# Kernel optimization log

Hardware: AMD Instinct MI355X
Metric: run time of the kernel (lower is better)

The kernel has to match this reference:

```python
import jax, jax.numpy as jnp
import numpy as np

MAX_DELAY = 48          # delay buffer depth
D1 = MAX_DELAY + 1
SIGMA = MAX_DELAY / 2.0
MAX_THINK = 8           # config.max_think_steps
NUM_CLASSES = 63
VOCAB = NUM_CLASSES + 1 # vocab includes think-end token
THINK_END = NUM_CLASSES
H = 512                 # hidden_size
B = 8                   # batch
T = 48                  # encoder time steps


def _calc_credit(tau):
    # relu(-|(d - clip(tau,1,D)) * (1/sigma)^2| + 1/sigma), shape (D1,H,H)
    tc = jnp.clip(tau, 1.0, float(MAX_DELAY))[None]
    d = jnp.arange(D1, dtype=tau.dtype)[:, None, None]
    inv = 1.0 / SIGMA
    return jax.nn.relu(inv - jnp.abs((d - tc) * (inv * inv)))


def _forward(x, wa, ba, lat, tau, we, be, N):
    cm = _calc_credit(tau) * lat[None]   # (D1,H,H), constant across steps
    d_idx = jnp.arange(D1)

    def step_b(buf, ptr, x_t):           # buf (D1,Bx,H), x_t (Bx,VOCAB)
        h_del = jax.lax.dynamic_index_in_dim(buf, ptr, 0, keepdims=False)
        h = jnp.tanh(x_t @ wa.T + ba + h_del)
        scat = jnp.einsum('dhi,bi->dbh', cm, h)
        shifted = scat[(d_idx - ptr) % D1]                      # roll by +ptr along d
        buf = (buf + shifted) * (d_idx != ptr).astype(buf.dtype)[:, None, None]
        y = h_del @ we.T + be
        return buf, (ptr + 1) % D1, y

    def step_1(buf, ptr, x_t):           # per-sample: buf (D1,H), x_t (VOCAB,)
        h_del = jax.lax.dynamic_index_in_dim(buf, ptr, 0, keepdims=False)
        h = jnp.tanh(wa @ x_t + ba + h_del)
        scat = jnp.einsum('dhi,i->dh', cm, h)
        shifted = scat[(d_idx - ptr) % D1]
        buf = (buf + shifted) * (d_idx != ptr).astype(buf.dtype)[:, None]
        y = we @ h_del + be
        return buf, (ptr + 1) % D1, y

    def gumbel_hard(y, k):               # F.gumbel_softmax(tau=1, hard=True)
        u = jax.random.uniform(k, y.shape, minval=1e-9, maxval=1.0)
        logits = y - jnp.log(-jnp.log(u))
        soft = jax.nn.softmax(logits)
        idx = jnp.argmax(logits)
        hard = jax.nn.one_hot(idx, VOCAB, dtype=y.dtype)
        return hard + soft - jax.lax.stop_gradient(soft), idx

    bsz = x.shape[0]
    buf0 = jnp.zeros((D1, bsz, H), x.dtype)

    def enc(carry, x_t):
        buf, ptr = carry
        buf, ptr, _ = step_b(buf, ptr, x_t)
        return (buf, ptr), None

    (buf, ptr), _ = jax.lax.scan(enc, (buf0, jnp.int32(0)), jnp.swapaxes(x, 0, 1))

    def decode_one(buf_i, x_last, key_i):
        # bounded think loop (original while-loop, max MAX_THINK+1 iterations)
        def think(carry, i):
            b, cur, p, done = carry
            nb, np_, y = step_1(b, p, cur)
            ncur, idx = gumbel_hard(y, jax.random.fold_in(key_i, i))
            b = jnp.where(done, b, nb)
            cur = jnp.where(done, cur, ncur)
            p = jnp.where(done, p, np_)
            done = done | (idx == THINK_END) | (i + 1 > MAX_THINK)
            return (b, cur, p, done), None
        (b, cur, p, _), _ = jax.lax.scan(
            think, (buf_i, x_last, ptr, jnp.bool_(False)), jnp.arange(MAX_THINK + 1))

        def dec(carry, j):
            b, cur, p = carry
            b, p, y = step_1(b, p, cur)
            ncur, _ = gumbel_hard(y, jax.random.fold_in(key_i, 10000 + j))
            return (b, ncur, p), y
        _, ys = jax.lax.scan(dec, (b, cur, p), jnp.arange(N))
        return ys                        # (N, VOCAB)

    keys = jax.random.split(jax.random.key(42), bsz)
    ys = jax.vmap(decode_one, in_axes=(1, 0, 0))(buf, x[:, -1, :], keys)
    return ys[:, :, :-1]                 # drop think-end logit


def setup_inputs() -> dict:
    key = jax.random.key(0)
    ks = jax.random.split(key, 6)
    x = jax.random.normal(ks[0], (B, T, VOCAB), dtype=jnp.float32)
    lim_a = (6.0 / (VOCAB + H)) ** 0.5
    w_afferent = jax.random.uniform(ks[1], (H, VOCAB), minval=-lim_a, maxval=lim_a)
    b_afferent = jnp.zeros((H,), jnp.float32)
    lim_l = (6.0 / (H + H)) ** 0.5
    lateral = jax.random.uniform(ks[2], (H, H), minval=-lim_l, maxval=lim_l)
    tau = MAX_DELAY * jax.random.uniform(ks[3], (H, H)) + 1.0
    lim_e = (6.0 / (H + VOCAB)) ** 0.5
    w_efferent = jax.random.uniform(ks[4], (VOCAB, H), minval=-lim_e, maxval=lim_e)
    b_efferent = jnp.zeros((VOCAB,), jnp.float32)
    return {"x": x, "w_afferent": w_afferent, "b_afferent": b_afferent,
            "lateral": lateral, "tau": tau,
            "w_efferent": w_efferent, "b_efferent": b_efferent, "N": T - 3}


def reference(x, w_afferent, b_afferent, lateral, tau, w_efferent, b_efferent, N):
    return _forward(x, w_afferent, b_afferent, lateral, tau, w_efferent, b_efferent, N)
```

## Files before the change

### kernel.cpp

```cpp
#include <hip/hip_runtime.h>
#include <stdint.h>

namespace {

constexpr int H = 512, V = 64, B = 8, T = 48, D1 = 49, NDEC = 45, NSTEP = 102;
constexpr int NBLK = 256, TPB = 512;
constexpr int NG = 8, GMEM = NBLK / NG;

constexpr size_t OFF_PUB  = 0;
constexpr size_t OFF_IDX  = 131072;
constexpr size_t OFF_PFLG = 132096;
constexpr size_t OFF_YPF  = 132352;
constexpr size_t OFF_YF   = 132416;
constexpr size_t OFF_BAR  = 132544;
constexpr size_t OFF_YP   = 133056;
constexpr size_t OFF_XW   = 149440;

__device__ __forceinline__ float ldA(const float* p) {
  return __hip_atomic_load(p, __ATOMIC_RELAXED, __HIP_MEMORY_SCOPE_AGENT);
}
__device__ __forceinline__ void stA(float* p, float v) {
  __hip_atomic_store(p, v, __ATOMIC_RELAXED, __HIP_MEMORY_SCOPE_AGENT);
}
__device__ __forceinline__ int ldAi(const int* p) {
  return __hip_atomic_load(p, __ATOMIC_RELAXED, __HIP_MEMORY_SCOPE_AGENT);
}
__device__ __forceinline__ void stAi(int* p, int v) {
  __hip_atomic_store(p, v, __ATOMIC_RELAXED, __HIP_MEMORY_SCOPE_AGENT);
}

__device__ __forceinline__ void tf2x32(uint32_t k0, uint32_t k1,
                                       uint32_t& x0, uint32_t& x1) {
  const uint32_t ks2 = k0 ^ k1 ^ 0x1BD11BDAu;
  x0 += k0; x1 += k1;
#define RR(r) { x0 += x1; x1 = (x1 << (r)) | (x1 >> (32-(r))); x1 ^= x0; }
  RR(13) RR(15) RR(26) RR(6)  x0 += k1;  x1 += ks2 + 1u;
  RR(17) RR(29) RR(16) RR(24) x0 += ks2; x1 += k0 + 2u;
  RR(13) RR(15) RR(26) RR(6)  x0 += k0;  x1 += k1 + 3u;
  RR(17) RR(29) RR(16) RR(24) x0 += k1;  x1 += ks2 + 4u;
  RR(13) RR(15) RR(26) RR(6)  x0 += ks2; x1 += k0 + 5u;
#undef RR
}

__device__ __forceinline__ float gumbel_from_bits(uint32_t bits) {
  float u = __uint_as_float((bits >> 9) | 0x3F800000u) - 1.0f;
  u = u + 1e-9f;
  return -logf(-logf(u));
}

__global__ __launch_bounds__(512) void k_zero(float* __restrict__ ws) {
  int* ib = (int*)ws;
  for (size_t i = OFF_PFLG + threadIdx.x; i < OFF_BAR + 512; i += 512)
    stAi(&ib[i], 0);
  for (int i = threadIdx.x; i < 32768; i += 512) stA(&ws[i], 0.0f);
}

__device__ __forceinline__ void gbar(int* bar, int grp, int ep) {
  asm volatile("s_waitcnt vmcnt(0)" ::: "memory");
  __syncthreads();
  if (threadIdx.x == 0) {
    int old = __hip_atomic_fetch_add(&bar[16 + 16 * grp], 1,
                                     __ATOMIC_RELAXED, __HIP_MEMORY_SCOPE_AGENT);
    if (((old + 1) & (GMEM - 1)) == 0) {
      int oldG = __hip_atomic_fetch_add(&bar[0], 1,
                                        __ATOMIC_RELAXED, __HIP_MEMORY_SCOPE_AGENT);
      if (((oldG + 1) & (NG - 1)) == 0) {
        #pragma unroll
        for (int q = 0; q < NG; ++q) stAi(&bar[160 + 16 * q], ep);
      }
    }
    int guard = 0;
    while (ldAi(&bar[160 + 16 * grp]) < ep) {
      __builtin_amdgcn_s_sleep(2);
      if (++guard > (1 << 20)) break;
    }
  }
  __syncthreads();
}

__global__ __launch_bounds__(TPB, 4)
void k_main(
    const float* __restrict__ x,  const float* __restrict__ wa,
    const float* __restrict__ ba, const float* __restrict__ lat,
    const float* __restrict__ tau,const float* __restrict__ we,
    const float* __restrict__ be, float* __restrict__ ws,
    float* __restrict__ out) {
  const int blk = blockIdx.x, tid = threadIdx.x;
  float* pub = ws + OFF_PUB;
  float* yp  = ws + OFF_YP;
  float* xw  = ws + OFF_XW;
  int* idxA  = (int*)ws + OFF_IDX;
  int* pflag = (int*)ws + OFF_PFLG;
  int* ypf   = (int*)ws + OFF_YPF;
  int* yf    = (int*)ws + OFF_YF;
  int* bar   = (int*)ws + OFF_BAR;

  const int p  = blk >> 5;
  const int g  = blk & 31;
  const int w  = tid >> 6, lane = tid & 63;
  const int cb = p * 64;
  const bool isG0  = (g == 0);
  const bool isFin = (g == 31);
  const int fb = p;

  __shared__ float s_h[8 * 64];
  __shared__ float s_hd2[8 * 64];
  __shared__ float s_tc[16 * 64];
  __shared__ float s_lat[16 * 64];
  __shared__ float s_buf[8 * 16 * 49];
  __shared__ int   s_ptr[8], s_cidx[8], s_done8[8];

  for (int q2 = tid; q2 < 8 * 16 * 49; q2 += TPB) s_buf[q2] = 0.0f;
  for (int q2 = tid; q2 < 16 * 64; q2 += TPB) {
    int hl = q2 >> 6, ii = q2 & 63;
    int ho = g * 16 + hl, i = cb + ii;
    float tv = tau[(size_t)ho * H + i];
    s_tc[q2]  = fminf(fmaxf(tv, 1.0f), 48.0f);
    s_lat[q2] = lat[(size_t)ho * H + i];
  }
  if (tid < 8) { s_ptr[tid] = 0; s_cidx[tid] = 0; s_done8[tid] = 0; }
  if (g < 24) {
    #pragma unroll
    for (int tt = 0; tt < 2; ++tt) {
      int t0 = g * 2 + tt;
      int b = (tid >> 6) & 7, il = tid & 63;
      int j = cb + il;
      const float* xr = x + ((size_t)b * T + t0) * V;
      const float* war = wa + (size_t)j * V;
      float acc = 0.0f;
      #pragma unroll
      for (int v = 0; v < V; v += 4) {
        float4 w4 = *(const float4*)(war + v);
        float4 x4 = *(const float4*)(xr + v);
        acc = fmaf(w4.x, x4.x, acc); acc = fmaf(w4.y, x4.y, acc);
        acc = fmaf(w4.z, x4.z, acc); acc = fmaf(w4.w, x4.w, acc);
      }
      stA(&xw[((size_t)t0 * 8 + b) * 512 + j], acc);
    }
  }
  uint32_t ka = 0u, kb = (uint32_t)fb;
  tf2x32(0u, 42u, ka, kb);

  gbar(bar, blk % NG, 1);

  for (int t = 0; t < NSTEP; ++t) {
    const bool thinkM = (t >= T && t < T + 9);
    const bool decM   = (t >= T + 9);
    const int needY   = (t - 1 >= T) ? 1 : 0;

    if (tid < 64) {
      int guard = 0;
      while (true) {
        int pred = 1;
        if (lane < 32)      pred = (ldAi(&pflag[p * 32 + lane]) >= t);
        else if (lane < 40 && needY) pred = (ldAi(&yf[lane - 32]) >= t - 1);
        if (__all(pred)) break;
        __builtin_amdgcn_s_sleep(1);
        if (++guard > (1 << 22)) break;
      }
    }
    __syncthreads();
    asm volatile("" ::: "memory");

    if (tid < 8 && t >= 1) {
      const int b = tid;
      const bool prevThink = (t - 1 >= T) && (t - 1 < T + 9);
      const bool aP = prevThink ? (s_done8[b] == 0) : true;
      if (t - 1 >= T) {
        int ix = ldAi(&idxA[(t - 1) * 8 + b]);
        if (aP) s_cidx[b] = ix;
        if (prevThink && (ix == 63 || (t - 1 - T) == 8)) s_done8[b] = 1;
      }
      if (aP) { int pv = s_ptr[b]; s_ptr[b] = (pv + 1 == D1) ? 0 : pv + 1; }
    }
    __syncthreads();

    int actM = 0;
    #pragma unroll
    for (int b = 0; b < B; ++b)
      actM |= ((thinkM ? (s_done8[b] ^ 1) : 1) & 1) << b;

    {
      int il = tid & 63, b = tid >> 6;
      int j = cb + il;
      const float* pr = pub + ((size_t)(t & 3) * 32768 + (size_t)j * 64 + b * 8);
      float p0 = ldA(pr),     p1 = ldA(pr + 1), p2 = ldA(pr + 2), p3 = ldA(pr + 3);
      float p4 = ldA(pr + 4), p5 = ldA(pr + 5), p6 = ldA(pr + 6), p7 = ldA(pr + 7);
      float hd = ((p0 + p1) + (p2 + p3)) + ((p4 + p5) + (p6 + p7));
      if (isG0 && t >= T) s_hd2[b * 64 + il] = hd;
      float acc;
      if (t <= T) {
        int xrow = (t < T) ? t : (T - 1);
        acc = (ba[j] + hd) + ldA(&xw[((size_t)xrow * 8 + b) * 512 + j]);
      } else {
        acc = (ba[j] + hd) + wa[(size_t)j * V + s_cidx[b]];
      }
      s_h[b * 64 + il] = tanhf(acc);
    }
    __syncthreads();

    if (isG0 && t >= T) {
      int b = tid >> 6, o = tid & 63;
      const float* wer = we + (size_t)o * H + cb;
      const float* hp  = &s_hd2[b * 64];
      float a2 = 0.0f;
      #pragma unroll
      for (int i2 = 0; i2 < 64; i2 += 4) {
        float4 w4 = *(const float4*)(wer + i2);
        a2 = fmaf(w4.x, hp[i2],     a2); a2 = fmaf(w4.y, hp[i2 + 1], a2);
        a2 = fmaf(w4.z, hp[i2 + 2], a2); a2 = fmaf(w4.w, hp[i2 + 3], a2);
      }
      stA(&yp[(size_t)(t & 3) * 4096 + (size_t)p * 512 + b * 64 + o], a2);
      asm volatile("s_waitcnt vmcnt(0)" ::: "memory");
      __syncthreads();
      if (tid == 0) stAi(&ypf[p], t);
    }

    {
      const float dd = (float)lane;
      const float inv = 1.0f / 24.0f, inv2 = inv * inv;
      float accA[8], accB[8];
      #pragma unroll
      for (int b = 0; b < B; ++b) { accA[b] = 0.0f; accB[b] = 0.0f; }
      const float* tcA = &s_tc[(w * 2) * 64];
      const float* ltA = &s_lat[(w * 2) * 64];
      const float* tcB = &s_tc[(w * 2 + 1) * 64];
      const float* ltB = &s_lat[(w * 2 + 1) * 64];
      #pragma unroll 4
      for (int ii = 0; ii < 64; ii += 4) {
        float4 tA = *(const float4*)(tcA + ii);
        float4 lA = *(const float4*)(ltA + ii);
        float4 tB = *(const float4*)(tcB + ii);
        float4 lB = *(const float4*)(ltB + ii);
        float qA[4], qB[4];
        #pragma unroll
        for (int k = 0; k < 4; ++k) {
          float ta = ((const float*)&tA)[k];
          qA[k] = fmaxf(0.0f, inv - fabsf((dd - ta) * inv2)) * ((const float*)&lA)[k];
          float tb = ((const float*)&tB)[k];
          qB[k] = fmaxf(0.0f, inv - fabsf((dd - tb) * inv2)) * ((const float*)&lB)[k];
        }
        #pragma unroll
        for (int b = 0; b < B; ++b) {
          float4 h4 = *(const float4*)(&s_h[b * 64 + ii]);
          const float* hp = (const float*)&h4;
          #pragma unroll
          for (int k = 0; k < 4; ++k) accA[b] = fmaf(qA[k], hp[k], accA[b]);
          #pragma unroll
          for (int k = 0; k < 4; ++k) accB[b] = fmaf(qB[k], hp[k], accB[b]);
        }
      }
      if (lane >= 1 && lane <= 48) {
        #pragma unroll
        for (int b = 0; b < B; ++b) {
          if ((actM >> b) & 1) {
            int slot = s_ptr[b] + lane; if (slot >= D1) slot -= D1;
            int aA = (b * 16 + w * 2) * 49 + slot;
            float oA = s_buf[aA];
            s_buf[aA] = (lane == 48) ? accA[b] : (oA + accA[b]);
            int aB = (b * 16 + w * 2 + 1) * 49 + slot;
            float oB = s_buf[aB];
            s_buf[aB] = (lane == 48) ? accB[b] : (oB + accB[b]);
          }
        }
      }
    }
    __syncthreads();

    if (tid < 128) {
      int hl = tid >> 3, b = tid & 7;
      int sn = ((actM >> b) & 1) ? s_ptr[b] + 1 : s_ptr[b];
      if (sn >= D1) sn -= D1;
      float val = s_buf[(b * 16 + hl) * 49 + sn];
      stA(&pub[(size_t)((t + 1) & 3) * 32768
               + (size_t)(g * 16 + hl) * 64 + b * 8 + p], val);
    }
    asm volatile("s_waitcnt vmcnt(0)" ::: "memory");
    __syncthreads();
    if (tid == 0) stAi(&pflag[g * 8 + p], t + 1);

    if (isFin && t >= T && tid < 64) {
      const int o = tid, it = t - T;
      if (o < 8) {
        int guard = 0;
        while (ldAi(&ypf[o]) < t) {
          __builtin_amdgcn_s_sleep(1);
          if (++guard > (1 << 22)) break;
        }
      }
      asm volatile("" ::: "memory");
      const float* ypr = yp + (size_t)(t & 3) * 4096 + fb * 64 + o;
      float y0 = ldA(ypr),        y1 = ldA(ypr + 512);
      float y2 = ldA(ypr + 1024), y3 = ldA(ypr + 1536);
      float y4 = ldA(ypr + 2048), y5 = ldA(ypr + 2560);
      float y6 = ldA(ypr + 3072), y7 = ldA(ypr + 3584);
      float y = (((y0 + y1) + (y2 + y3)) + ((y4 + y5) + (y6 + y7))) + be[o];
      if (decM && o < V - 1)
        out[((size_t)fb * NDEC + (t - T - 9)) * (V - 1) + o] = y;
      uint32_t data = (it < 9) ? (uint32_t)it : (uint32_t)(10000 + (it - 9));
      uint32_t e = 0u, f = data; tf2x32(ka, kb, e, f);
      uint32_t r0 = 0u, r1 = (uint32_t)o; tf2x32(e, f, r0, r1);
      float bv = y + gumbel_from_bits(r0 ^ r1);
      int bi = o;
      #pragma unroll
      for (int m = 32; m >= 1; m >>= 1) {
        float ov = __shfl_xor(bv, m, 64);
        int   oi = __shfl_xor(bi, m, 64);
        if (ov > bv || (ov == bv && oi < bi)) { bv = ov; bi = oi; }
      }
      if (o == 0) {
        stAi(&idxA[t * 8 + fb], bi);
        asm volatile("s_waitcnt vmcnt(0)" ::: "memory");
        stAi(&yf[fb], t);
      }
    }
  }
}

}

extern "C" void kernel_launch(void* const* d_in, const int* in_sizes, int n_in,
                              void* d_out, int out_size, void* d_ws, size_t ws_size,
                              hipStream_t stream) {
  (void)in_sizes; (void)n_in; (void)out_size; (void)ws_size;
  const float* x   = (const float*)d_in[0];
  const float* wa  = (const float*)d_in[1];
  const float* ba  = (const float*)d_in[2];
  const float* lat = (const float*)d_in[3];
  const float* tau = (const float*)d_in[4];
  const float* we  = (const float*)d_in[5];
  const float* be  = (const float*)d_in[6];
  float* out = (float*)d_out;
  float* ws  = (float*)d_ws;

  k_zero<<<dim3(1), dim3(512), 0, stream>>>(ws);
  k_main<<<dim3(NBLK), dim3(TPB), 0, stream>>>(x, wa, ba, lat, tau, we, be, ws, out);
}
```

Before: 1.596 ms.

## Publish next-step delay slot early from wave 0 and move decode work to wave 1

Wave 0 now snapshots the next delayed-state slot and computes its delay-1 credit contribution directly, so it can publish to other blocks and raise the progress flag before the full 48-slot scatter finishes. Wave 1 takes over the efferent projection and the final gumbel/argmax decode, running concurrently with the scatter instead of after extra block barriers. This shortens the critical path of the cross-block recurrence. The cost is duplicated delay-1 arithmetic and more divergent per-wave work.

```diff
diff --git a/kernel.cpp b/kernel.cpp
--- a/kernel.cpp
+++ b/kernel.cpp
@@ -108,6 +108,7 @@
   __shared__ float s_tc[16 * 64];
   __shared__ float s_lat[16 * 64];
   __shared__ float s_buf[8 * 16 * 49];
+  __shared__ float s_snap[128];
   __shared__ int   s_ptr[8], s_cidx[8], s_done8[8];
 
   for (int q2 = tid; q2 < 8 * 16 * 49; q2 += TPB) s_buf[q2] = 0.0f;
@@ -197,23 +198,104 @@
       }
       s_h[b * 64 + il] = tanhf(acc);
     }
+    if (tid < 128) {
+      int hl = tid >> 3, b = tid & 7;
+      int sn = ((actM >> b) & 1) ? s_ptr[b] + 1 : s_ptr[b];
+      if (sn >= D1) sn -= D1;
+      s_snap[tid] = s_buf[(b * 16 + hl) * 49 + sn];
+    }
     __syncthreads();
 
-    if (isG0 && t >= T) {
-      int b = tid >> 6, o = tid & 63;
-      const float* wer = we + (size_t)o * H + cb;
-      const float* hp  = &s_hd2[b * 64];
-      float a2 = 0.0f;
+    if (w == 0) {
+      const float dd = 1.0f;
+      const float inv = 1.0f / 24.0f, inv2 = inv * inv;
       #pragma unroll
-      for (int i2 = 0; i2 < 64; i2 += 4) {
-        float4 w4 = *(const float4*)(wer + i2);
-        a2 = fmaf(w4.x, hp[i2],     a2); a2 = fmaf(w4.y, hp[i2 + 1], a2);
-        a2 = fmaf(w4.z, hp[i2 + 2], a2); a2 = fmaf(w4.w, hp[i2 + 3], a2);
-      }
-      stA(&yp[(size_t)(t & 3) * 4096 + (size_t)p * 512 + b * 64 + o], a2);
+      for (int half = 0; half < 2; ++half) {
+        int m = lane + half * 64;
+        int hl = m >> 3, b = m & 7;
+        float val = s_snap[m];
+        if ((actM >> b) & 1) {
+          float acc = 0.0f;
+          const float* tcr = &s_tc[hl * 64];
+          const float* ltr = &s_lat[hl * 64];
+          const float* hr  = &s_h[b * 64];
+          #pragma unroll 4
+          for (int ii = 0; ii < 64; ii += 4) {
+            float4 t4 = *(const float4*)(tcr + ii);
+            float4 l4 = *(const float4*)(ltr + ii);
+            float4 h4 = *(const float4*)(hr + ii);
+            float q0 = fmaxf(0.0f, inv - fabsf((dd - t4.x) * inv2)) * l4.x;
+            acc = fmaf(q0, h4.x, acc);
+            float q1 = fmaxf(0.0f, inv - fabsf((dd - t4.y) * inv2)) * l4.y;
+            acc = fmaf(q1, h4.y, acc);
+            float q2 = fmaxf(0.0f, inv - fabsf((dd - t4.z) * inv2)) * l4.z;
+            acc = fmaf(q2, h4.z, acc);
+            float q3 = fmaxf(0.0f, inv - fabsf((dd - t4.w) * inv2)) * l4.w;
+            acc = fmaf(q3, h4.w, acc);
+          }
+          val = val + acc;
+        }
+        stA(&pub[(size_t)((t + 1) & 3) * 32768
+                 + (size_t)(g * 16 + hl) * 64 + b * 8 + p], val);
+      }
       asm volatile("s_waitcnt vmcnt(0)" ::: "memory");
-      __syncthreads();
-      if (tid == 0) stAi(&ypf[p], t);
+      if (lane == 0) stAi(&pflag[g * 8 + p], t + 1);
+    }
+
+    if (w == 1) {
+      if (isG0 && t >= T) {
+        int o = lane;
+        const float* wer = we + (size_t)o * H + cb;
+        #pragma unroll
+        for (int b = 0; b < 8; ++b) {
+          const float* hp = &s_hd2[b * 64];
+          float a2 = 0.0f;
+          #pragma unroll 4
+          for (int i2 = 0; i2 < 64; i2 += 4) {
+            float4 w4 = *(const float4*)(wer + i2);
+            a2 = fmaf(w4.x, hp[i2],     a2); a2 = fmaf(w4.y, hp[i2 + 1], a2);
+            a2 = fmaf(w4.z, hp[i2 + 2], a2); a2 = fmaf(w4.w, hp[i2 + 3], a2);
+          }
+          stA(&yp[(size_t)(t & 3) * 4096 + (size_t)p * 512 + b * 64 + o], a2);
+        }
+        asm volatile("s_waitcnt vmcnt(0)" ::: "memory");
+        if (lane == 0) stAi(&ypf[p], t);
+      }
+      if (isFin && t >= T) {
+        const int o = lane, it = t - T;
+        if (o < 8) {
+          int guard = 0;
+          while (ldAi(&ypf[o]) < t) {
+            __builtin_amdgcn_s_sleep(1);
+            if (++guard > (1 << 22)) break;
+          }
+        }
+        asm volatile("" ::: "memory");
+        const float* ypr = yp + (size_t)(t & 3) * 4096 + fb * 64 + o;
+        float y0 = ldA(ypr),        y1 = ldA(ypr + 512);
+        float y2 = ldA(ypr + 1024), y3 = ldA(ypr + 1536);
+        float y4 = ldA(ypr + 2048), y5 = ldA(ypr + 2560);
+        float y6 = ldA(ypr + 3072), y7 = ldA(ypr + 3584);
+        float y = (((y0 + y1) + (y2 + y3)) + ((y4 + y5) + (y6 + y7))) + be[o];
+        if (decM && o < V - 1)
+          out[((size_t)fb * NDEC + (t - T - 9)) * (V - 1) + o] = y;
+        uint32_t data = (it < 9) ? (uint32_t)it : (uint32_t)(10000 + (it - 9));
+        uint32_t e = 0u, f = data; tf2x32(ka, kb, e, f);
+        uint32_t r0 = 0u, r1 = (uint32_t)o; tf2x32(e, f, r0, r1);
+        float bv = y + gumbel_from_bits(r0 ^ r1);
+        int bi = o;
+        #pragma unroll
+        for (int m2 = 32; m2 >= 1; m2 >>= 1) {
+          float ov = __shfl_xor(bv, m2, 64);
+          int   oi = __shfl_xor(bi, m2, 64);
+          if (ov > bv || (ov == bv && oi < bi)) { bv = ov; bi = oi; }
+        }
+        if (o == 0) {
+          stAi(&idxA[t * 8 + fb], bi);
+          asm volatile("s_waitcnt vmcnt(0)" ::: "memory");
+          stAi(&yf[fb], t);
+        }
+      }
     }
 
     {
@@ -266,54 +348,6 @@
       }
     }
     __syncthreads();
-
-    if (tid < 128) {
-      int hl = tid >> 3, b = tid & 7;
-      int sn = ((actM >> b) & 1) ? s_ptr[b] + 1 : s_ptr[b];
-      if (sn >= D1) sn -= D1;
-      float val = s_buf[(b * 16 + hl) * 49 + sn];
-      stA(&pub[(size_t)((t + 1) & 3) * 32768
-               + (size_t)(g * 16 + hl) * 64 + b * 8 + p], val);
-    }
-    asm volatile("s_waitcnt vmcnt(0)" ::: "memory");
-    __syncthreads();
-    if (tid == 0) stAi(&pflag[g * 8 + p], t + 1);
-
-    if (isFin && t >= T && tid < 64) {
-      const int o = tid, it = t - T;
-      if (o < 8) {
-        int guard = 0;
-        while (ldAi(&ypf[o]) < t) {
-          __builtin_amdgcn_s_sleep(1);
-          if (++guard > (1 << 22)) break;
-        }
-      }
-      asm volatile("" ::: "memory");
-      const float* ypr = yp + (size_t)(t & 3) * 4096 + fb * 64 + o;
-      float y0 = ldA(ypr),        y1 = ldA(ypr + 512);
-      float y2 = ldA(ypr + 1024), y3 = ldA(ypr + 1536);
-      float y4 = ldA(ypr + 2048), y5 = ldA(ypr + 2560);
-      float y6 = ldA(ypr + 3072), y7 = ldA(ypr + 3584);
-      float y = (((y0 + y1) + (y2 + y3)) + ((y4 + y5) + (y6 + y7))) + be[o];
-      if (decM && o < V - 1)
-        out[((size_t)fb * NDEC + (t - T - 9)) * (V - 1) + o] = y;
-      uint32_t data = (it < 9) ? (uint32_t)it : (uint32_t)(10000 + (it - 9));
-      uint32_t e = 0u, f = data; tf2x32(ka, kb, e, f);
-      uint32_t r0 = 0u, r1 = (uint32_t)o; tf2x32(e, f, r0, r1);
-      float bv = y + gumbel_from_bits(r0 ^ r1);
-      int bi = o;
-      #pragma unroll
-      for (int m = 32; m >= 1; m >>= 1) {
-        float ov = __shfl_xor(bv, m, 64);
-        int   oi = __shfl_xor(bi, m, 64);
-        if (ov > bv || (ov == bv && oi < bi)) { bv = ov; bi = oi; }
-      }
-      if (o == 0) {
-        stAi(&idxA[t * 8 + fb], bi);
-        asm volatile("s_waitcnt vmcnt(0)" ::: "memory");
-        stAi(&yf[fb], t);
-      }
-    }
   }
 }
 
```

Measured after the change: 1.608 ms. About the same (+0.7%).

## Split recurrent work over twice as many smaller blocks and defer output projection

Applied to the files above, without the earlier changes.

Doubles the grid to 512 blocks of 256 threads, so each block owns 8 hidden rows instead of 16. This shrinks per-block shared memory and the per-step lateral scatter work. The flag array and workspace offsets are resized to match, and the yf wait moves to a separate wave. The efferent partial-logit computation in group-0 blocks now runs after the step's state is published and its flag set, taking it off the critical path of the recurrence. The cost is more blocks taking part in the spin-wait synchronisation each step, with more flags to poll.

```diff
diff --git a/kernel.cpp b/kernel.cpp
--- a/kernel.cpp
+++ b/kernel.cpp
@@ -4,17 +4,17 @@
 namespace {
 
 constexpr int H = 512, V = 64, B = 8, T = 48, D1 = 49, NDEC = 45, NSTEP = 102;
-constexpr int NBLK = 256, TPB = 512;
+constexpr int NBLK = 512, TPB = 256;
 constexpr int NG = 8, GMEM = NBLK / NG;
 
 constexpr size_t OFF_PUB  = 0;
 constexpr size_t OFF_IDX  = 131072;
 constexpr size_t OFF_PFLG = 132096;
-constexpr size_t OFF_YPF  = 132352;
-constexpr size_t OFF_YF   = 132416;
-constexpr size_t OFF_BAR  = 132544;
-constexpr size_t OFF_YP   = 133056;
-constexpr size_t OFF_XW   = 149440;
+constexpr size_t OFF_YPF  = 132608;
+constexpr size_t OFF_YF   = 132672;
+constexpr size_t OFF_BAR  = 132736;
+constexpr size_t OFF_YP   = 133248;
+constexpr size_t OFF_XW   = 149632;
 
 __device__ __forceinline__ float ldA(const float* p) {
   return __hip_atomic_load(p, __ATOMIC_RELAXED, __HIP_MEMORY_SCOPE_AGENT);
@@ -95,37 +95,37 @@
   int* yf    = (int*)ws + OFF_YF;
   int* bar   = (int*)ws + OFF_BAR;
 
-  const int p  = blk >> 5;
-  const int g  = blk & 31;
+  const int p  = blk >> 6;
+  const int g  = blk & 63;
   const int w  = tid >> 6, lane = tid & 63;
   const int cb = p * 64;
   const bool isG0  = (g == 0);
-  const bool isFin = (g == 31);
+  const bool isFin = (g == 63);
   const int fb = p;
 
   __shared__ float s_h[8 * 64];
   __shared__ float s_hd2[8 * 64];
-  __shared__ float s_tc[16 * 64];
-  __shared__ float s_lat[16 * 64];
-  __shared__ float s_buf[8 * 16 * 49];
+  __shared__ float s_tc[8 * 64];
+  __shared__ float s_lat[8 * 64];
+  __shared__ float s_buf[8 * 8 * 49];
   __shared__ int   s_ptr[8], s_cidx[8], s_done8[8];
 
-  for (int q2 = tid; q2 < 8 * 16 * 49; q2 += TPB) s_buf[q2] = 0.0f;
-  for (int q2 = tid; q2 < 16 * 64; q2 += TPB) {
+  for (int q2 = tid; q2 < 8 * 8 * 49; q2 += TPB) s_buf[q2] = 0.0f;
+  for (int q2 = tid; q2 < 8 * 64; q2 += TPB) {
     int hl = q2 >> 6, ii = q2 & 63;
-    int ho = g * 16 + hl, i = cb + ii;
+    int ho = g * 8 + hl, i = cb + ii;
     float tv = tau[(size_t)ho * H + i];
     s_tc[q2]  = fminf(fmaxf(tv, 1.0f), 48.0f);
     s_lat[q2] = lat[(size_t)ho * H + i];
   }
   if (tid < 8) { s_ptr[tid] = 0; s_cidx[tid] = 0; s_done8[tid] = 0; }
-  if (g < 24) {
+  if (g < T) {
+    int il = tid & 63, b0 = tid >> 6;
+    int j = cb + il;
     #pragma unroll
-    for (int tt = 0; tt < 2; ++tt) {
-      int t0 = g * 2 + tt;
-      int b = (tid >> 6) & 7, il = tid & 63;
-      int j = cb + il;
-      const float* xr = x + ((size_t)b * T + t0) * V;
+    for (int half = 0; half < 2; ++half) {
+      int b = b0 + half * 4;
+      const float* xr = x + ((size_t)b * T + g) * V;
       const float* war = wa + (size_t)j * V;
       float acc = 0.0f;
       #pragma unroll
@@ -135,13 +135,13 @@
         acc = fmaf(w4.x, x4.x, acc); acc = fmaf(w4.y, x4.y, acc);
         acc = fmaf(w4.z, x4.z, acc); acc = fmaf(w4.w, x4.w, acc);
       }
-      stA(&xw[((size_t)t0 * 8 + b) * 512 + j], acc);
+      stA(&xw[((size_t)g * 8 + b) * 512 + j], acc);
     }
   }
   uint32_t ka = 0u, kb = (uint32_t)fb;
   tf2x32(0u, 42u, ka, kb);
 
-  gbar(bar, blk % NG, 1);
+  gbar(bar, blk & 7, 1);
 
   for (int t = 0; t < NSTEP; ++t) {
     const bool thinkM = (t >= T && t < T + 9);
@@ -151,10 +151,14 @@
     if (tid < 64) {
       int guard = 0;
       while (true) {
-        int pred = 1;
-        if (lane < 32)      pred = (ldAi(&pflag[p * 32 + lane]) >= t);
-        else if (lane < 40 && needY) pred = (ldAi(&yf[lane - 32]) >= t - 1);
+        int pred = (ldAi(&pflag[p * 64 + tid]) >= t) ? 1 : 0;
         if (__all(pred)) break;
+        __builtin_amdgcn_s_sleep(1);
+        if (++guard > (1 << 22)) break;
+      }
+    } else if (tid >= 64 && tid < 72 && needY) {
+      int guard = 0;
+      while (ldAi(&yf[tid - 64]) < t - 1) {
         __builtin_amdgcn_s_sleep(1);
         if (++guard > (1 << 22)) break;
       }
@@ -181,40 +185,27 @@
       actM |= ((thinkM ? (s_done8[b] ^ 1) : 1) & 1) << b;
 
     {
-      int il = tid & 63, b = tid >> 6;
+      int il = tid & 63, b0 = tid >> 6;
       int j = cb + il;
-      const float* pr = pub + ((size_t)(t & 3) * 32768 + (size_t)j * 64 + b * 8);
-      float p0 = ldA(pr),     p1 = ldA(pr + 1), p2 = ldA(pr + 2), p3 = ldA(pr + 3);
-      float p4 = ldA(pr + 4), p5 = ldA(pr + 5), p6 = ldA(pr + 6), p7 = ldA(pr + 7);
-      float hd = ((p0 + p1) + (p2 + p3)) + ((p4 + p5) + (p6 + p7));
-      if (isG0 && t >= T) s_hd2[b * 64 + il] = hd;
-      float acc;
-      if (t <= T) {
-        int xrow = (t < T) ? t : (T - 1);
-        acc = (ba[j] + hd) + ldA(&xw[((size_t)xrow * 8 + b) * 512 + j]);
-      } else {
-        acc = (ba[j] + hd) + wa[(size_t)j * V + s_cidx[b]];
-      }
-      s_h[b * 64 + il] = tanhf(acc);
-    }
-    __syncthreads();
-
-    if (isG0 && t >= T) {
-      int b = tid >> 6, o = tid & 63;
-      const float* wer = we + (size_t)o * H + cb;
-      const float* hp  = &s_hd2[b * 64];
-      float a2 = 0.0f;
-      #pragma unroll
-      for (int i2 = 0; i2 < 64; i2 += 4) {
-        float4 w4 = *(const float4*)(wer + i2);
-        a2 = fmaf(w4.x, hp[i2],     a2); a2 = fmaf(w4.y, hp[i2 + 1], a2);
-        a2 = fmaf(w4.z, hp[i2 + 2], a2); a2 = fmaf(w4.w, hp[i2 + 3], a2);
-      }
-      stA(&yp[(size_t)(t & 3) * 4096 + (size_t)p * 512 + b * 64 + o], a2);
-      asm volatile("s_waitcnt vmcnt(0)" ::: "memory");
-      __syncthreads();
-      if (tid == 0) stAi(&ypf[p], t);
-    }
+      #pragma unroll
+      for (int half = 0; half < 2; ++half) {
+        int b = b0 + half * 4;
+        const float* pr = pub + ((size_t)(t & 3) * 32768 + (size_t)j * 64 + b * 8);
+        float p0 = ldA(pr),     p1 = ldA(pr + 1), p2 = ldA(pr + 2), p3 = ldA(pr + 3);
+        float p4 = ldA(pr + 4), p5 = ldA(pr + 5), p6 = ldA(pr + 6), p7 = ldA(pr + 7);
+        float hd = ((p0 + p1) + (p2 + p3)) + ((p4 + p5) + (p6 + p7));
+        if (isG0 && t >= T) s_hd2[b * 64 + il] = hd;
+        float acc;
+        if (t <= T) {
+          int xrow = (t < T) ? t : (T - 1);
+          acc = (ba[j] + hd) + ldA(&xw[((size_t)xrow * 8 + b) * 512 + j]);
+        } else {
+          acc = (ba[j] + hd) + wa[(size_t)j * V + s_cidx[b]];
+        }
+        s_h[b * 64 + il] = tanhf(acc);
+      }
+    }
+    __syncthreads();
 
     {
       const float dd = (float)lane;
@@ -255,10 +246,10 @@
         for (int b = 0; b < B; ++b) {
           if ((actM >> b) & 1) {
             int slot = s_ptr[b] + lane; if (slot >= D1) slot -= D1;
-            int aA = (b * 16 + w * 2) * 49 + slot;
+            int aA = (b * 8 + w * 2) * 49 + slot;
             float oA = s_buf[aA];
             s_buf[aA] = (lane == 48) ? accA[b] : (oA + accA[b]);
-            int aB = (b * 16 + w * 2 + 1) * 49 + slot;
+            int aB = (b * 8 + w * 2 + 1) * 49 + slot;
             float oB = s_buf[aB];
             s_buf[aB] = (lane == 48) ? accB[b] : (oB + accB[b]);
           }
@@ -267,18 +258,38 @@
     }
     __syncthreads();
 
-    if (tid < 128) {
+    if (tid < 64) {
       int hl = tid >> 3, b = tid & 7;
       int sn = ((actM >> b) & 1) ? s_ptr[b] + 1 : s_ptr[b];
       if (sn >= D1) sn -= D1;
-      float val = s_buf[(b * 16 + hl) * 49 + sn];
+      float val = s_buf[(b * 8 + hl) * 49 + sn];
       stA(&pub[(size_t)((t + 1) & 3) * 32768
-               + (size_t)(g * 16 + hl) * 64 + b * 8 + p], val);
+               + (size_t)(g * 8 + hl) * 64 + b * 8 + p], val);
     }
     asm volatile("s_waitcnt vmcnt(0)" ::: "memory");
     __syncthreads();
     if (tid == 0) stAi(&pflag[g * 8 + p], t + 1);
 
+    if (isG0 && t >= T) {
+      int o = tid & 63, b0 = tid >> 6;
+      const float* wer = we + (size_t)o * H + cb;
+      #pragma unroll
+      for (int half = 0; half < 2; ++half) {
+        int b = b0 + half * 4;
+        const float* hp = &s_hd2[b * 64];
+        float a2 = 0.0f;
+        #pragma unroll 4
+        for (int i2 = 0; i2 < 64; i2 += 4) {
+          float4 w4 = *(const float4*)(wer + i2);
+          a2 = fmaf(w4.x, hp[i2],     a2); a2 = fmaf(w4.y, hp[i2 + 1], a2);
+          a2 = fmaf(w4.z, hp[i2 + 2], a2); a2 = fmaf(w4.w, hp[i2 + 3], a2);
+        }
+        stA(&yp[(size_t)(t & 3) * 4096 + (size_t)p * 512 + b * 64 + o], a2);
+      }
+      asm volatile("s_waitcnt vmcnt(0)" ::: "memory");
+      __syncthreads();
+      if (tid == 0) stAi(&ypf[p], t);
+    }
     if (isFin && t >= T && tid < 64) {
       const int o = tid, it = t - T;
       if (o < 8) {
@@ -303,9 +314,9 @@
       float bv = y + gumbel_from_bits(r0 ^ r1);
       int bi = o;
       #pragma unroll
-      for (int m = 32; m >= 1; m >>= 1) {
-        float ov = __shfl_xor(bv, m, 64);
-        int   oi = __shfl_xor(bi, m, 64);
+      for (int m2 = 32; m2 >= 1; m2 >>= 1) {
+        float ov = __shfl_xor(bv, m2, 64);
+        int   oi = __shfl_xor(bi, m2, 64);
         if (ov > bv || (ov == bv && oi < bi)) { bv = ov; bi = oi; }
       }
       if (o == 0) {
```

Measured after the change: 2.343 ms. +46.8%, slower.
